# Performance work log

Hardware: AMD Instinct MI355X
Metric: run time of the kernel (lower is better)

## Reference

```python
import jax, jax.numpy as jnp
import numpy as np

T = 8
TAU = 2.0
V_TH = 1.0
V_RESET = 0.0
ALPHA = 2.0  # ATan surrogate alpha

@jax.custom_vjp
def spike(v):
    # Heaviside(v) with ATan surrogate gradient
    return (v >= 0.0).astype(v.dtype)

def _spike_fwd(v):
    return spike(v), v

def _spike_bwd(v, g):
    sg = (ALPHA / 2.0) / (1.0 + (jnp.pi / 2.0 * ALPHA * v) ** 2)
    return (g * sg,)

spike.defvjp(_spike_fwd, _spike_bwd)

def conv2d(x, w):
    return jax.lax.conv_general_dilated(x, w, (1, 1), 'SAME',
                                        dimension_numbers=('NCHW', 'OIHW', 'NCHW'))

def batchnorm(x, g, b, m, v):
    # inference-mode BN over channel dim of NCHW
    scale = (g / jnp.sqrt(v + 1e-5))[None, :, None, None]
    return (x - m[None, :, None, None]) * scale + b[None, :, None, None]

def maxpool2(x):
    return jax.lax.reduce_window(x, -jnp.inf, jax.lax.max,
                                 (1, 1, 2, 2), (1, 1, 2, 2), 'VALID')

def if_scan(x_seq):
    # x_seq: [T, ...]; IF neuron: v += x; spike; hard reset
    def step(v, x_t):
        v = v + x_t
        s = spike(v - V_TH)
        v = v * (1.0 - s) + V_RESET * s
        return v, s
    v0 = jnp.full_like(x_seq[0], V_RESET)
    _, s_seq = jax.lax.scan(step, v0, x_seq)
    return s_seq

def lif_scan(x_seq):
    # LIF neuron: v += (x - (v - v_reset)) / tau; spike; hard reset
    def step(v, x_t):
        v = v + (x_t - (v - V_RESET)) / TAU
        s = spike(v - V_TH)
        v = v * (1.0 - s) + V_RESET * s
        return v, s
    v0 = jnp.full_like(x_seq[0], V_RESET)
    _, s_seq = jax.lax.scan(step, v0, x_seq)
    return s_seq

def setup_inputs() -> dict:
    key = jax.random.key(0)
    ks = jax.random.split(key, 6)
    B = 64
    d = {
        'x': jax.random.normal(ks[0], (B, 1, 28, 28), dtype=jnp.float32),
        'conv1_w': jax.random.normal(ks[1], (128, 1, 3, 3), dtype=jnp.float32) * 0.3,
        'bn1_g': jnp.ones((128,), jnp.float32),
        'bn1_b': jnp.zeros((128,), jnp.float32),
        'bn1_m': jnp.zeros((128,), jnp.float32),
        'bn1_v': jnp.ones((128,), jnp.float32),
        'conv2_w': jax.random.normal(ks[2], (128, 128, 3, 3), dtype=jnp.float32) * 0.05,
        'bn2_g': jnp.ones((128,), jnp.float32),
        'bn2_b': jnp.zeros((128,), jnp.float32),
        'bn2_m': jnp.zeros((128,), jnp.float32),
        'bn2_v': jnp.ones((128,), jnp.float32),
        'fc1_w': jax.random.normal(ks[3], (128 * 3 * 3, 128 * 7 * 7), dtype=jnp.float32) * 0.02,
        'fc2_w': jax.random.normal(ks[4], (128, 128 * 3 * 3), dtype=jnp.float32) * 0.05,
        'fc3_w': jax.random.normal(ks[5], (10, 128), dtype=jnp.float32) * 0.1,
    }
    return d

def reference(x, conv1_w, bn1_g, bn1_b, bn1_m, bn1_v,
              conv2_w, bn2_g, bn2_b, bn2_m, bn2_v,
              fc1_w, fc2_w, fc3_w):
    B = x.shape[0]
    # static conv + BN (applied once, repeated T times)
    y0 = batchnorm(conv2d(x, conv1_w), bn1_g, bn1_b, bn1_m, bn1_v)  # [B,128,28,28]
    x_seq = jnp.broadcast_to(y0, (T,) + y0.shape)
    s1 = if_scan(x_seq)  # [T,B,128,28,28]
    # pool -> conv -> BN per timestep (vectorized over T*B)
    h = s1.reshape((T * B, 128, 28, 28))
    h = maxpool2(h)                       # [TB,128,14,14]
    h = batchnorm(conv2d(h, conv2_w), bn2_g, bn2_b, bn2_m, bn2_v)
    s2 = if_scan(h.reshape((T, B, 128, 14, 14)))
    # pool -> flatten (dropout is identity in eval mode)
    h = maxpool2(s2.reshape((T * B, 128, 14, 14)))  # [TB,128,7,7]
    h = h.reshape((T, B, 128 * 7 * 7))
    h = jnp.einsum('tbi,oi->tbo', h, fc1_w)   # [T,B,1152]
    s3 = lif_scan(h)
    h = jnp.einsum('tbi,oi->tbo', s3, fc2_w)  # [T,B,128]
    s4 = lif_scan(h)
    h = jnp.einsum('tbi,oi->tbo', s4, fc3_w)  # [T,B,10]
    s5 = lif_scan(h)
    return s5.sum(0) / T
```

## Files before the change

### kernel.cpp

```cpp
#include <hip/hip_runtime.h>
#include <hip/hip_bf16.h>
#include <cstddef>


typedef __attribute__((ext_vector_type(8))) short  short8;
typedef __attribute__((ext_vector_type(4))) float  f32x4;
typedef __attribute__((ext_vector_type(8))) __bf16 bf16x8;

__device__ inline short f2bf_bits(float x) {
    __hip_bfloat16 h = __float2bfloat16(x);
    return *reinterpret_cast<short*>(&h);
}
__device__ inline float bfbits2f(short b) {
    __hip_bfloat16 h;
    *reinterpret_cast<short*>(&h) = b;
    return __bfloat162float(h);
}

__global__ __launch_bounds__(256) void prep2_kernel(
    const float* __restrict__ w2, const float* __restrict__ g2,
    const float* __restrict__ v2, __hip_bfloat16* __restrict__ w2s,
    float* __restrict__ sc2)
{
    int id = blockIdx.x * 256 + threadIdx.x;
    if (id < 128) sc2[id] = g2[id] / sqrtf(v2[id] + 1e-5f);
    int ci = id & 127;
    int co = (id >> 7) & 127;
    int k  = id >> 14;
    float w  = w2[(co * 128 + ci) * 9 + k];
    float hi = __bfloat162float(__float2bfloat16(w));
    float r1 = w - hi;
    float md = __bfloat162float(__float2bfloat16(r1));
    float r2 = r1 - md;
    size_t base = ((size_t)k * 128 + co) * 128 + ci;
    const size_t SPL = 9 * 128 * 128;
    w2s[0 * SPL + base] = __float2bfloat16(hi);
    w2s[1 * SPL + base] = __float2bfloat16(md);
    w2s[2 * SPL + base] = __float2bfloat16(r2);
}

__global__ __launch_bounds__(256) void prep_fc1_kernel(
    const float* __restrict__ w, short* __restrict__ w1s)
{
    int id = blockIdx.x * 256 + threadIdx.x;
    int koct = id % 784;
    int n    = id / 784;
    const float* src = w + (size_t)n * 6272 + koct * 8;
    float4 va = *(const float4*)src;
    float4 vb = *(const float4*)(src + 4);
    float wv[8] = {va.x, va.y, va.z, va.w, vb.x, vb.y, vb.z, vb.w};
    short8 hi8, md8, lo8;
#pragma unroll
    for (int e = 0; e < 8; ++e) {
        float x  = wv[e];
        short hb = f2bf_bits(x);
        float r1 = x - bfbits2f(hb);
        short mb = f2bf_bits(r1);
        float r2 = r1 - bfbits2f(mb);
        hi8[e] = hb; md8[e] = mb; lo8[e] = f2bf_bits(r2);
    }
    const size_t SPL = (size_t)1152 * 6272;
    size_t base = (size_t)n * 6272 + koct * 8;
    *(short8*)&w1s[0 * SPL + base] = hi8;
    *(short8*)&w1s[1 * SPL + base] = md8;
    *(short8*)&w1s[2 * SPL + base] = lo8;
}

__global__ __launch_bounds__(256) void stage1_kernel(
    const float* __restrict__ x,  const float* __restrict__ w1,
    const float* __restrict__ g1, const float* __restrict__ b1,
    const float* __restrict__ m1, const float* __restrict__ v1,
    __hip_bfloat16* __restrict__ p1bf)
{
    int id = blockIdx.x * 256 + threadIdx.x;
    int c  = id & 127;
    int bp = id >> 7;
    int p  = bp % 196;
    int b  = bp / 196;
    int ph = p / 14, pw = p % 14;

    float scale = g1[c] / sqrtf(v1[c] + 1e-5f);
    float mu = m1[c], beta = b1[c];
    float wl[9];
#pragma unroll
    for (int k = 0; k < 9; ++k) wl[k] = w1[c * 9 + k];

    const float* xb = x + b * 784;
    float y[4];
#pragma unroll
    for (int i = 0; i < 4; ++i) {
        int h = 2 * ph + (i >> 1);
        int w = 2 * pw + (i & 1);
        float acc = 0.f;
#pragma unroll
        for (int kh = 0; kh < 3; ++kh) {
#pragma unroll
            for (int kw = 0; kw < 3; ++kw) {
                int hh = h + kh - 1, ww = w + kw - 1;
                if ((unsigned)hh < 28u && (unsigned)ww < 28u)
                    acc += xb[hh * 28 + ww] * wl[kh * 3 + kw];
            }
        }
        y[i] = (acc - mu) * scale + beta;
    }

    float v0 = 0.f, v1m = 0.f, v2m = 0.f, v3m = 0.f;
#pragma unroll
    for (int t = 0; t < 8; ++t) {
        float any = 0.f;
        v0  += y[0]; if (v0  >= 1.0f) { any = 1.0f; v0  = 0.0f; }
        v1m += y[1]; if (v1m >= 1.0f) { any = 1.0f; v1m = 0.0f; }
        v2m += y[2]; if (v2m >= 1.0f) { any = 1.0f; v2m = 0.0f; }
        v3m += y[3]; if (v3m >= 1.0f) { any = 1.0f; v3m = 0.0f; }
        p1bf[((size_t)(t * 64 + b) * 196 + p) * 128 + c] = __float2bfloat16(any);
    }
}

__global__ __launch_bounds__(256, 2) void conv2m_kernel(
    const short* __restrict__ p1bf, const short* __restrict__ w2s,
    const float* __restrict__ sc2,  const float* __restrict__ b2,
    const float* __restrict__ m2,   float* __restrict__ a2t)
{
    __shared__ short patch[272 * 128];
    int bx   = blockIdx.x;
    int tb   = bx >> 1;
    int ch   = bx & 1;
    int tid  = threadIdx.x;
    int lane = tid & 63;
    int wv   = tid >> 6;
    int wm   = wv >> 1, wn = wv & 1;
    int l15  = lane & 15, lg = lane >> 4;

    const short8 z8 = {0, 0, 0, 0, 0, 0, 0, 0};
    for (int idx = tid; idx < 76 * 16; idx += 256) {
        int cell = idx >> 4, sl = idx & 15;
        int prow, pcol;
        if (cell < 48) {
            int g = cell >> 4;
            prow = (g == 0) ? 0 : ((g == 1) ? 15 : 16);
            pcol = cell & 15;
        } else {
            int e = cell - 48;
            prow = 1 + (e >> 1);
            pcol = (e & 1) ? 15 : 0;
        }
        *(short8*)&patch[(prow * 16 + pcol) * 128 + sl * 8] = z8;
    }
    const short* src = p1bf + (size_t)tb * (196 * 128);
    for (int idx = tid; idx < 196 * 16; idx += 256) {
        int pos = idx >> 4, q = idx & 15;
        short8 v = *(const short8*)&src[pos * 128 + q * 8];
        int h = pos / 14, w = pos - h * 14;
        int lpos = (h + 1) * 16 + (w + 1);
        *(short8*)&patch[lpos * 128 + (q ^ (lpos & 15)) * 8] = v;
    }
    __syncthreads();

    int abase[7];
#pragma unroll
    for (int mi = 0; mi < 7; ++mi) {
        int pos = (wm * 6 + mi) * 16 + l15;
        int r = pos / 14, c = pos - r * 14;
        abase[mi] = r * 16 + c;
    }
    int co0 = ch * 64 + wn * 32;

    f32x4 acc[7][2];
#pragma unroll
    for (int mi = 0; mi < 7; ++mi) {
        acc[mi][0] = (f32x4){0.f, 0.f, 0.f, 0.f};
        acc[mi][1] = (f32x4){0.f, 0.f, 0.f, 0.f};
    }

    const size_t SPL = 9 * 128 * 128;
    for (int chunk = 0; chunk < 4; ++chunk) {
#pragma unroll
        for (int tap = 0; tap < 9; ++tap) {
            const int t16 = (tap / 3) * 16 + (tap % 3);
            short8 bfr[3][2];
#pragma unroll
            for (int s = 0; s < 3; ++s)
#pragma unroll
                for (int nt = 0; nt < 2; ++nt)
                    bfr[s][nt] = *(const short8*)&w2s[s * SPL +
                        ((size_t)tap * 128 + co0 + nt * 16 + l15) * 128 + chunk * 32 + lg * 8];
#pragma unroll
            for (int mi = 0; mi < 7; ++mi) {
                int lpos = abase[mi] + t16;
                short8 av = *(const short8*)&patch[lpos * 128 +
                                                   (((chunk * 4 + lg) ^ (lpos & 15)) * 8)];
                if (wm == 1 && mi == 6 && l15 >= 4) av = z8;
                bf16x8 a = __builtin_bit_cast(bf16x8, av);
#pragma unroll
                for (int s = 0; s < 3; ++s)
#pragma unroll
                    for (int nt = 0; nt < 2; ++nt)
                        acc[mi][nt] = __builtin_amdgcn_mfma_f32_16x16x32_bf16(
                            a, __builtin_bit_cast(bf16x8, bfr[s][nt]), acc[mi][nt], 0, 0, 0);
            }
        }
    }

    float scv[2], mv[2], bv[2];
#pragma unroll
    for (int nt = 0; nt < 2; ++nt) {
        int co = co0 + nt * 16 + l15;
        scv[nt] = sc2[co]; mv[nt] = m2[co]; bv[nt] = b2[co];
    }
#pragma unroll
    for (int mi = 0; mi < 7; ++mi) {
        int mt = wm * 6 + mi;
#pragma unroll
        for (int nt = 0; nt < 2; ++nt) {
            int co = co0 + nt * 16 + l15;
#pragma unroll
            for (int reg = 0; reg < 4; ++reg) {
                int pos = mt * 16 + lg * 4 + reg;
                if (pos < 196)
                    a2t[((size_t)tb * 196 + pos) * 128 + co] =
                        (acc[mi][nt][reg] - mv[nt]) * scv[nt] + bv[nt];
            }
        }
    }
}

__global__ __launch_bounds__(256) void stage2_kernel(
    const float* __restrict__ a2t, __hip_bfloat16* __restrict__ p2)
{
    int id = blockIdx.x * 256 + threadIdx.x;
    int c  = id & 127;
    int bp = id >> 7;
    int p  = bp % 49;
    int b  = bp / 49;
    int ph = p / 7, pw = p % 7;
    int s0 = (2 * ph) * 14 + 2 * pw;

    float v0 = 0.f, v1 = 0.f, v2 = 0.f, v3 = 0.f;
#pragma unroll
    for (int t = 0; t < 8; ++t) {
        const float* base = a2t + ((size_t)(t * 64 + b) * 196) * 128 + c;
        float x0 = base[(s0) * 128],      x1 = base[(s0 + 1) * 128];
        float x2 = base[(s0 + 14) * 128], x3 = base[(s0 + 15) * 128];
        float any = 0.f;
        v0 += x0; if (v0 >= 1.0f) { any = 1.0f; v0 = 0.0f; }
        v1 += x1; if (v1 >= 1.0f) { any = 1.0f; v1 = 0.0f; }
        v2 += x2; if (v2 >= 1.0f) { any = 1.0f; v2 = 0.0f; }
        v3 += x3; if (v3 >= 1.0f) { any = 1.0f; v3 = 0.0f; }
        p2[(size_t)(t * 64 + b) * 6272 + c * 49 + p] = __float2bfloat16(any);
    }
}

__global__ __launch_bounds__(256, 2) void fc1m_kernel(
    const short* __restrict__ A,
    const short* __restrict__ Bsp,
    float* __restrict__ part)
{
    __shared__ short At[64 * 64];
    const int n0 = blockIdx.x * 128;
    const int m0 = blockIdx.y * 64;
    const int kz = blockIdx.z;
    const int tid  = threadIdx.x;
    const int lane = tid & 63;
    const int wv   = tid >> 6;
    const int wm = wv >> 1, wn = wv & 1;
    const int l15 = lane & 15, lg = lane >> 4;
    const size_t SPL = (size_t)1152 * 6272;

    f32x4 acc[2][4];
#pragma unroll
    for (int mi = 0; mi < 2; ++mi)
#pragma unroll
        for (int nt = 0; nt < 4; ++nt)
            acc[mi][nt] = (f32x4){0.f, 0.f, 0.f, 0.f};

    for (int ks = 0; ks < 14; ++ks) {
        int k0 = kz * 896 + ks * 64;
#pragma unroll
        for (int pp = 0; pp < 2; ++pp) {
            int i = pp * 256 + tid;
            int row = i >> 3, q = i & 7;
            short8 v = *(const short8*)&A[(size_t)(m0 + row) * 6272 + k0 + ((q ^ (row & 7)) << 3)];
            *(short8*)&At[row * 64 + q * 8] = v;
        }
        __syncthreads();

#pragma unroll
        for (int kh = 0; kh < 2; ++kh) {
            bf16x8 a[2];
#pragma unroll
            for (int mi = 0; mi < 2; ++mi) {
                int r = wm * 32 + mi * 16 + l15;
                int q = (kh * 4 + lg) ^ (r & 7);
                a[mi] = __builtin_bit_cast(bf16x8, *(const short8*)&At[r * 64 + q * 8]);
            }
#pragma unroll
            for (int s = 0; s < 3; ++s) {
#pragma unroll
                for (int nt = 0; nt < 4; ++nt) {
                    bf16x8 b = __builtin_bit_cast(bf16x8, *(const short8*)&Bsp[s * SPL +
                        (size_t)(n0 + wn * 64 + nt * 16 + l15) * 6272 + k0 + kh * 32 + lg * 8]);
                    acc[0][nt] = __builtin_amdgcn_mfma_f32_16x16x32_bf16(a[0], b, acc[0][nt], 0, 0, 0);
                    acc[1][nt] = __builtin_amdgcn_mfma_f32_16x16x32_bf16(a[1], b, acc[1][nt], 0, 0, 0);
                }
            }
        }
        __syncthreads();
    }

    float* dst = part + (size_t)kz * (512 * 1152);
#pragma unroll
    for (int mi = 0; mi < 2; ++mi) {
#pragma unroll
        for (int nt = 0; nt < 4; ++nt) {
            int n = n0 + wn * 64 + nt * 16 + l15;
#pragma unroll
            for (int reg = 0; reg < 4; ++reg) {
                int m = m0 + wm * 32 + mi * 16 + lg * 4 + reg;
                dst[(size_t)m * 1152 + n] = acc[mi][nt][reg];
            }
        }
    }
}

__global__ __launch_bounds__(256) void lif2_kernel(
    const float* __restrict__ part, float* __restrict__ s3)
{
    int id = blockIdx.x * 256 + threadIdx.x;
    int f = id % 1152;
    int b = id / 1152;
    const size_t S = (size_t)512 * 1152;
    float v = 0.f;
#pragma unroll
    for (int t = 0; t < 8; ++t) {
        size_t off = (size_t)(t * 64 + b) * 1152 + f;
        float x = part[off];
#pragma unroll
        for (int s = 1; s < 7; ++s) x += part[s * S + off];
        v = v + (x - v) * 0.5f;
        s3[off] = (v >= 1.0f) ? 1.0f : 0.0f;
        if (v >= 1.0f) v = 0.0f;
    }
}

__global__ __launch_bounds__(256) void gemm_nt_kernel(
    const float* __restrict__ A, const float* __restrict__ Bw,
    float* __restrict__ C, int M, int N, int K)
{
    __shared__ float As[16][36];
    __shared__ float Bs[16][68];
    int m_base = blockIdx.y * 32;
    int n_base = blockIdx.x * 64;
    int tid = threadIdx.x;
    int tx = tid & 15, ty = tid >> 4;
    float acc[2][4] = {{0.f,0.f,0.f,0.f},{0.f,0.f,0.f,0.f}};

    for (int k0 = 0; k0 < K; k0 += 16) {
        if (tid < 128) {
            int m  = tid >> 2;
            int kk = (tid & 3) << 2;
            float4 av = *(const float4*)&A[(size_t)(m_base + m) * K + k0 + kk];
            As[kk + 0][m] = av.x; As[kk + 1][m] = av.y;
            As[kk + 2][m] = av.z; As[kk + 3][m] = av.w;
        }
        {
            int n  = tid >> 2;
            int kk = (tid & 3) << 2;
            float4 bv = *(const float4*)&Bw[(size_t)(n_base + n) * K + k0 + kk];
            Bs[kk + 0][n] = bv.x; Bs[kk + 1][n] = bv.y;
            Bs[kk + 2][n] = bv.z; Bs[kk + 3][n] = bv.w;
        }
        __syncthreads();
#pragma unroll
        for (int kk = 0; kk < 16; ++kk) {
            float a0 = As[kk][ty * 2 + 0];
            float a1 = As[kk][ty * 2 + 1];
            float4 bv = *(const float4*)&Bs[kk][tx * 4];
            acc[0][0] += a0 * bv.x; acc[0][1] += a0 * bv.y;
            acc[0][2] += a0 * bv.z; acc[0][3] += a0 * bv.w;
            acc[1][0] += a1 * bv.x; acc[1][1] += a1 * bv.y;
            acc[1][2] += a1 * bv.z; acc[1][3] += a1 * bv.w;
        }
        __syncthreads();
    }
#pragma unroll
    for (int i = 0; i < 2; ++i) {
        float4 r;
        r.x = acc[i][0]; r.y = acc[i][1]; r.z = acc[i][2]; r.w = acc[i][3];
        *(float4*)&C[(size_t)(m_base + ty * 2 + i) * N + n_base + tx * 4] = r;
    }
}

__global__ __launch_bounds__(128) void tail_kernel(
    const float* __restrict__ h2, const float* __restrict__ w3,
    float* __restrict__ out)
{
    __shared__ float st[8][128];
    __shared__ float dd[8][10];
    int b = blockIdx.x;
    int tid = threadIdx.x;
    float v = 0.f;
#pragma unroll
    for (int t = 0; t < 8; ++t) {
        float x = h2[(size_t)(t * 64 + b) * 128 + tid];
        v = v + (x - v) * 0.5f;
        st[t][tid] = (v >= 1.0f) ? 1.0f : 0.0f;
        if (v >= 1.0f) v = 0.0f;
    }
    __syncthreads();
    if (tid < 80) {
        int t = tid / 10, o = tid - (tid / 10) * 10;
        float dot = 0.f;
        for (int k = 0; k < 128; ++k) dot += st[t][k] * w3[o * 128 + k];
        dd[t][o] = dot;
    }
    __syncthreads();
    if (tid < 10) {
        float vv = 0.f, cnt = 0.f;
#pragma unroll
        for (int t = 0; t < 8; ++t) {
            float x = dd[t][tid];
            vv = vv + (x - vv) * 0.5f;
            if (vv >= 1.0f) { cnt += 1.0f; vv = 0.0f; }
        }
        out[b * 10 + tid] = cnt * 0.125f;
    }
}

extern "C" void kernel_launch(void* const* d_in, const int* in_sizes, int n_in,
                              void* d_out, int out_size, void* d_ws, size_t ws_size,
                              hipStream_t stream)
{
    (void)in_sizes; (void)n_in; (void)out_size; (void)ws_size;
    const float* x    = (const float*)d_in[0];
    const float* w1   = (const float*)d_in[1];
    const float* g1   = (const float*)d_in[2];
    const float* b1   = (const float*)d_in[3];
    const float* m1   = (const float*)d_in[4];
    const float* v1   = (const float*)d_in[5];
    const float* w2   = (const float*)d_in[6];
    const float* g2   = (const float*)d_in[7];
    const float* b2   = (const float*)d_in[8];
    const float* m2   = (const float*)d_in[9];
    const float* v2   = (const float*)d_in[10];
    const float* fc1w = (const float*)d_in[11];
    const float* fc2w = (const float*)d_in[12];
    const float* fc3w = (const float*)d_in[13];
    float* out = (float*)d_out;

    char* ws = (char*)d_ws;
    __hip_bfloat16* p1bf = (__hip_bfloat16*)(ws + 0);
    float*          a2t  = (float*)(ws + 25690112);
    __hip_bfloat16* w2s  = (__hip_bfloat16*)(ws + 77070336);
    float*          sc2  = (float*)(ws + 77955072);
    __hip_bfloat16* p2bf = (__hip_bfloat16*)(ws + 0);
    float*          part = (float*)(ws + 6422528);
    float*          s3   = (float*)(ws + 22937600);
    float*          h2   = (float*)(ws + 25296896);
    short*          w1s  = (short*)(ws + 25690112);

    prep2_kernel  <<<576,  256, 0, stream>>>(w2, g2, v2, w2s, sc2);
    stage1_kernel <<<6272, 256, 0, stream>>>(x, w1, g1, b1, m1, v1, p1bf);
    conv2m_kernel <<<1024, 256, 0, stream>>>((const short*)p1bf, (const short*)w2s,
                                             sc2, b2, m2, a2t);
    stage2_kernel <<<1568, 256, 0, stream>>>(a2t, p2bf);
    prep_fc1_kernel<<<3528, 256, 0, stream>>>(fc1w, w1s);
    fc1m_kernel   <<<dim3(9, 8, 7), 256, 0, stream>>>((const short*)p2bf, w1s, part);
    lif2_kernel   <<<288,  256, 0, stream>>>(part, s3);
    gemm_nt_kernel<<<dim3(2, 16), 256, 0, stream>>>(s3, fc2w, h2, 512, 128, 1152);
    tail_kernel   <<<64,   128, 0, stream>>>(h2, fc3w, out);
}
```

Before: 466.2 us.

## Halve conv2 LDS tile, swap fc1 grid order, fuse fc2 GEMM with LIF tail

The conv2 kernel now stages the input patch in two 64-channel halves, halving shared memory so the occupancy hint can rise from 2 to 4 blocks per SM. It swaps the XOR swizzle to use 8 slots. The fc1 grid is transposed so adjacent blocks walk M instead of N, which changes L2 reuse of the weights. The fp32 fc2 GEMM and the tail kernel are replaced by one fused kernel per batch element that reads bf16 spikes and does a 3-way bf16 split of fc2 weights on MFMA. That removes a launch and the h2 round trip, but the conversion is redone in every block.

Result: faster. 439.1 us (-5.8%).

```diff
diff --git a/kernel.cpp b/kernel.cpp
--- a/kernel.cpp
+++ b/kernel.cpp
@@ -116,12 +116,12 @@
     }
 }
 
-__global__ __launch_bounds__(256, 2) void conv2m_kernel(
+__global__ __launch_bounds__(256, 4) void conv2m_kernel(
     const short* __restrict__ p1bf, const short* __restrict__ w2s,
     const float* __restrict__ sc2,  const float* __restrict__ b2,
     const float* __restrict__ m2,   float* __restrict__ a2t)
 {
-    __shared__ short patch[272 * 128];
+    __shared__ short patch[272 * 64];
     int bx   = blockIdx.x;
     int tb   = bx >> 1;
     int ch   = bx & 1;
@@ -132,8 +132,8 @@
     int l15  = lane & 15, lg = lane >> 4;
 
     const short8 z8 = {0, 0, 0, 0, 0, 0, 0, 0};
-    for (int idx = tid; idx < 76 * 16; idx += 256) {
-        int cell = idx >> 4, sl = idx & 15;
+    for (int idx = tid; idx < 76 * 8; idx += 256) {
+        int cell = idx >> 3, q = idx & 7;
         int prow, pcol;
         if (cell < 48) {
             int g = cell >> 4;
@@ -144,24 +144,16 @@
             prow = 1 + (e >> 1);
             pcol = (e & 1) ? 15 : 0;
         }
-        *(short8*)&patch[(prow * 16 + pcol) * 128 + sl * 8] = z8;
-    }
-    const short* src = p1bf + (size_t)tb * (196 * 128);
-    for (int idx = tid; idx < 196 * 16; idx += 256) {
-        int pos = idx >> 4, q = idx & 15;
-        short8 v = *(const short8*)&src[pos * 128 + q * 8];
-        int h = pos / 14, w = pos - h * 14;
-        int lpos = (h + 1) * 16 + (w + 1);
-        *(short8*)&patch[lpos * 128 + (q ^ (lpos & 15)) * 8] = v;
-    }
-    __syncthreads();
-
-    int abase[7];
+        *(short8*)&patch[(prow * 16 + pcol) * 64 + q * 8] = z8;
+    }
+
+    int abase[7], pbase[7];
 #pragma unroll
     for (int mi = 0; mi < 7; ++mi) {
         int pos = (wm * 6 + mi) * 16 + l15;
         int r = pos / 14, c = pos - r * 14;
         abase[mi] = r * 16 + c;
+        pbase[mi] = pos;
     }
     int co0 = ch * 64 + wn * 32;
 
@@ -172,31 +164,47 @@
         acc[mi][1] = (f32x4){0.f, 0.f, 0.f, 0.f};
     }
 
+    const short* src = p1bf + (size_t)tb * (196 * 128);
     const size_t SPL = 9 * 128 * 128;
-    for (int chunk = 0; chunk < 4; ++chunk) {
-#pragma unroll
-        for (int tap = 0; tap < 9; ++tap) {
-            const int t16 = (tap / 3) * 16 + (tap % 3);
-            short8 bfr[3][2];
-#pragma unroll
-            for (int s = 0; s < 3; ++s)
-#pragma unroll
-                for (int nt = 0; nt < 2; ++nt)
-                    bfr[s][nt] = *(const short8*)&w2s[s * SPL +
-                        ((size_t)tap * 128 + co0 + nt * 16 + l15) * 128 + chunk * 32 + lg * 8];
-#pragma unroll
-            for (int mi = 0; mi < 7; ++mi) {
-                int lpos = abase[mi] + t16;
-                short8 av = *(const short8*)&patch[lpos * 128 +
-                                                   (((chunk * 4 + lg) ^ (lpos & 15)) * 8)];
-                if (wm == 1 && mi == 6 && l15 >= 4) av = z8;
-                bf16x8 a = __builtin_bit_cast(bf16x8, av);
+
+    for (int half = 0; half < 2; ++half) {
+        if (half) __syncthreads();
+        for (int idx = tid; idx < 196 * 8; idx += 256) {
+            int pos = idx >> 3, q = idx & 7;
+            short8 v = *(const short8*)&src[pos * 128 + half * 64 + q * 8];
+            int h = pos / 14, w = pos - h * 14;
+            int lpos = (h + 1) * 16 + (w + 1);
+            *(short8*)&patch[lpos * 64 + ((q ^ (pos & 7)) << 3)] = v;
+        }
+        __syncthreads();
+
+        for (int c2 = 0; c2 < 2; ++c2) {
+            int cibase = half * 64 + c2 * 32;
+#pragma unroll
+            for (int tap = 0; tap < 9; ++tap) {
+                const int t16 = (tap / 3) * 16 + (tap % 3);
+                const int tc  = (tap / 3 - 1) * 14 + (tap % 3) - 1;
+                short8 bfr[3][2];
 #pragma unroll
                 for (int s = 0; s < 3; ++s)
 #pragma unroll
                     for (int nt = 0; nt < 2; ++nt)
-                        acc[mi][nt] = __builtin_amdgcn_mfma_f32_16x16x32_bf16(
-                            a, __builtin_bit_cast(bf16x8, bfr[s][nt]), acc[mi][nt], 0, 0, 0);
+                        bfr[s][nt] = *(const short8*)&w2s[s * SPL +
+                            ((size_t)tap * 128 + co0 + nt * 16 + l15) * 128 + cibase + lg * 8];
+#pragma unroll
+                for (int mi = 0; mi < 7; ++mi) {
+                    int lpos = abase[mi] + t16;
+                    int q2 = (c2 * 4 + lg) ^ ((pbase[mi] + tc) & 7);
+                    short8 av = *(const short8*)&patch[lpos * 64 + q2 * 8];
+                    if (wm == 1 && mi == 6 && l15 >= 4) av = z8;
+                    bf16x8 a = __builtin_bit_cast(bf16x8, av);
+#pragma unroll
+                    for (int s = 0; s < 3; ++s)
+#pragma unroll
+                        for (int nt = 0; nt < 2; ++nt)
+                            acc[mi][nt] = __builtin_amdgcn_mfma_f32_16x16x32_bf16(
+                                a, __builtin_bit_cast(bf16x8, bfr[s][nt]), acc[mi][nt], 0, 0, 0);
+                }
             }
         }
     }
@@ -256,8 +264,8 @@
     float* __restrict__ part)
 {
     __shared__ short At[64 * 64];
-    const int n0 = blockIdx.x * 128;
-    const int m0 = blockIdx.y * 64;
+    const int m0 = blockIdx.x * 64;
+    const int n0 = blockIdx.y * 128;
     const int kz = blockIdx.z;
     const int tid  = threadIdx.x;
     const int lane = tid & 63;
@@ -323,7 +331,7 @@
 }
 
 __global__ __launch_bounds__(256) void lif2_kernel(
-    const float* __restrict__ part, float* __restrict__ s3)
+    const float* __restrict__ part, __hip_bfloat16* __restrict__ s3)
 {
     int id = blockIdx.x * 256 + threadIdx.x;
     int f = id % 1152;
@@ -337,80 +345,84 @@
 #pragma unroll
         for (int s = 1; s < 7; ++s) x += part[s * S + off];
         v = v + (x - v) * 0.5f;
-        s3[off] = (v >= 1.0f) ? 1.0f : 0.0f;
+        s3[off] = __float2bfloat16((v >= 1.0f) ? 1.0f : 0.0f);
         if (v >= 1.0f) v = 0.0f;
     }
 }
 
-__global__ __launch_bounds__(256) void gemm_nt_kernel(
-    const float* __restrict__ A, const float* __restrict__ Bw,
-    float* __restrict__ C, int M, int N, int K)
-{
-    __shared__ float As[16][36];
-    __shared__ float Bs[16][68];
-    int m_base = blockIdx.y * 32;
-    int n_base = blockIdx.x * 64;
-    int tid = threadIdx.x;
-    int tx = tid & 15, ty = tid >> 4;
-    float acc[2][4] = {{0.f,0.f,0.f,0.f},{0.f,0.f,0.f,0.f}};
-
-    for (int k0 = 0; k0 < K; k0 += 16) {
-        if (tid < 128) {
-            int m  = tid >> 2;
-            int kk = (tid & 3) << 2;
-            float4 av = *(const float4*)&A[(size_t)(m_base + m) * K + k0 + kk];
-            As[kk + 0][m] = av.x; As[kk + 1][m] = av.y;
-            As[kk + 2][m] = av.z; As[kk + 3][m] = av.w;
-        }
-        {
-            int n  = tid >> 2;
-            int kk = (tid & 3) << 2;
-            float4 bv = *(const float4*)&Bw[(size_t)(n_base + n) * K + k0 + kk];
-            Bs[kk + 0][n] = bv.x; Bs[kk + 1][n] = bv.y;
-            Bs[kk + 2][n] = bv.z; Bs[kk + 3][n] = bv.w;
-        }
-        __syncthreads();
-#pragma unroll
-        for (int kk = 0; kk < 16; ++kk) {
-            float a0 = As[kk][ty * 2 + 0];
-            float a1 = As[kk][ty * 2 + 1];
-            float4 bv = *(const float4*)&Bs[kk][tx * 4];
-            acc[0][0] += a0 * bv.x; acc[0][1] += a0 * bv.y;
-            acc[0][2] += a0 * bv.z; acc[0][3] += a0 * bv.w;
-            acc[1][0] += a1 * bv.x; acc[1][1] += a1 * bv.y;
-            acc[1][2] += a1 * bv.z; acc[1][3] += a1 * bv.w;
-        }
-        __syncthreads();
-    }
-#pragma unroll
-    for (int i = 0; i < 2; ++i) {
-        float4 r;
-        r.x = acc[i][0]; r.y = acc[i][1]; r.z = acc[i][2]; r.w = acc[i][3];
-        *(float4*)&C[(size_t)(m_base + ty * 2 + i) * N + n_base + tx * 4] = r;
-    }
-}
-
-__global__ __launch_bounds__(128) void tail_kernel(
-    const float* __restrict__ h2, const float* __restrict__ w3,
+__global__ __launch_bounds__(256) void fc2tail_kernel(
+    const short* __restrict__ s3bf,
+    const float* __restrict__ fc2w,
+    const float* __restrict__ fc3w,
     float* __restrict__ out)
 {
-    __shared__ float st[8][128];
+    __shared__ float h2[8][128];
+    __shared__ float s4[8][128];
     __shared__ float dd[8][10];
-    int b = blockIdx.x;
-    int tid = threadIdx.x;
-    float v = 0.f;
-#pragma unroll
-    for (int t = 0; t < 8; ++t) {
-        float x = h2[(size_t)(t * 64 + b) * 128 + tid];
-        v = v + (x - v) * 0.5f;
-        st[t][tid] = (v >= 1.0f) ? 1.0f : 0.0f;
-        if (v >= 1.0f) v = 0.0f;
+    int b    = blockIdx.x;
+    int tid  = threadIdx.x;
+    int lane = tid & 63;
+    int wv   = tid >> 6;
+    int l15  = lane & 15, lg = lane >> 4;
+
+    const short8 z8 = {0, 0, 0, 0, 0, 0, 0, 0};
+    f32x4 acc[2] = {(f32x4){0.f, 0.f, 0.f, 0.f}, (f32x4){0.f, 0.f, 0.f, 0.f}};
+
+    for (int ks = 0; ks < 36; ++ks) {
+        short8 av = (l15 < 8)
+            ? *(const short8*)&s3bf[(size_t)(l15 * 64 + b) * 1152 + ks * 32 + lg * 8]
+            : z8;
+        bf16x8 a = __builtin_bit_cast(bf16x8, av);
+#pragma unroll
+        for (int nt = 0; nt < 2; ++nt) {
+            int o = wv * 32 + nt * 16 + l15;
+            const float* wp = &fc2w[(size_t)o * 1152 + ks * 32 + lg * 8];
+            float4 wa = *(const float4*)wp;
+            float4 wb = *(const float4*)(wp + 4);
+            float wvv[8] = {wa.x, wa.y, wa.z, wa.w, wb.x, wb.y, wb.z, wb.w};
+            short8 hi8, md8, lo8;
+#pragma unroll
+            for (int e = 0; e < 8; ++e) {
+                float xw = wvv[e];
+                short hb = f2bf_bits(xw);
+                float r1 = xw - bfbits2f(hb);
+                short mb = f2bf_bits(r1);
+                float r2 = r1 - bfbits2f(mb);
+                hi8[e] = hb; md8[e] = mb; lo8[e] = f2bf_bits(r2);
+            }
+            acc[nt] = __builtin_amdgcn_mfma_f32_16x16x32_bf16(
+                a, __builtin_bit_cast(bf16x8, hi8), acc[nt], 0, 0, 0);
+            acc[nt] = __builtin_amdgcn_mfma_f32_16x16x32_bf16(
+                a, __builtin_bit_cast(bf16x8, md8), acc[nt], 0, 0, 0);
+            acc[nt] = __builtin_amdgcn_mfma_f32_16x16x32_bf16(
+                a, __builtin_bit_cast(bf16x8, lo8), acc[nt], 0, 0, 0);
+        }
+    }
+#pragma unroll
+    for (int nt = 0; nt < 2; ++nt) {
+#pragma unroll
+        for (int reg = 0; reg < 4; ++reg) {
+            int t = lg * 4 + reg;
+            if (t < 8) h2[t][wv * 32 + nt * 16 + l15] = acc[nt][reg];
+        }
+    }
+    __syncthreads();
+
+    if (tid < 128) {
+        float v = 0.f;
+#pragma unroll
+        for (int t = 0; t < 8; ++t) {
+            float xv = h2[t][tid];
+            v = v + (xv - v) * 0.5f;
+            s4[t][tid] = (v >= 1.0f) ? 1.0f : 0.0f;
+            if (v >= 1.0f) v = 0.0f;
+        }
     }
     __syncthreads();
     if (tid < 80) {
         int t = tid / 10, o = tid - (tid / 10) * 10;
         float dot = 0.f;
-        for (int k = 0; k < 128; ++k) dot += st[t][k] * w3[o * 128 + k];
+        for (int k = 0; k < 128; ++k) dot += s4[t][k] * fc3w[o * 128 + k];
         dd[t][o] = dot;
     }
     __syncthreads();
@@ -418,8 +430,8 @@
         float vv = 0.f, cnt = 0.f;
 #pragma unroll
         for (int t = 0; t < 8; ++t) {
-            float x = dd[t][tid];
-            vv = vv + (x - vv) * 0.5f;
+            float xv = dd[t][tid];
+            vv = vv + (xv - vv) * 0.5f;
             if (vv >= 1.0f) { cnt += 1.0f; vv = 0.0f; }
         }
         out[b * 10 + tid] = cnt * 0.125f;
@@ -454,18 +466,16 @@
     float*          sc2  = (float*)(ws + 77955072);
     __hip_bfloat16* p2bf = (__hip_bfloat16*)(ws + 0);
     float*          part = (float*)(ws + 6422528);
-    float*          s3   = (float*)(ws + 22937600);
-    float*          h2   = (float*)(ws + 25296896);
+    __hip_bfloat16* s3bf = (__hip_bfloat16*)(ws + 22937600);
     short*          w1s  = (short*)(ws + 25690112);
 
-    prep2_kernel  <<<576,  256, 0, stream>>>(w2, g2, v2, w2s, sc2);
-    stage1_kernel <<<6272, 256, 0, stream>>>(x, w1, g1, b1, m1, v1, p1bf);
-    conv2m_kernel <<<1024, 256, 0, stream>>>((const short*)p1bf, (const short*)w2s,
-                                             sc2, b2, m2, a2t);
-    stage2_kernel <<<1568, 256, 0, stream>>>(a2t, p2bf);
+    prep2_kernel   <<<576,  256, 0, stream>>>(w2, g2, v2, w2s, sc2);
+    stage1_kernel  <<<6272, 256, 0, stream>>>(x, w1, g1, b1, m1, v1, p1bf);
+    conv2m_kernel  <<<1024, 256, 0, stream>>>((const short*)p1bf, (const short*)w2s,
+                                              sc2, b2, m2, a2t);
+    stage2_kernel  <<<1568, 256, 0, stream>>>(a2t, p2bf);
     prep_fc1_kernel<<<3528, 256, 0, stream>>>(fc1w, w1s);
-    fc1m_kernel   <<<dim3(9, 8, 7), 256, 0, stream>>>((const short*)p2bf, w1s, part);
-    lif2_kernel   <<<288,  256, 0, stream>>>(part, s3);
-    gemm_nt_kernel<<<dim3(2, 16), 256, 0, stream>>>(s3, fc2w, h2, 512, 128, 1152);
-    tail_kernel   <<<64,   128, 0, stream>>>(h2, fc3w, out);
-}
+    fc1m_kernel    <<<dim3(8, 9, 7), 256, 0, stream>>>((const short*)p2bf, w1s, part);
+    lif2_kernel    <<<288,  256, 0, stream>>>(part, s3bf);
+    fc2tail_kernel <<<64,   256, 0, stream>>>((const short*)s3bf, fc2w, fc3w, out);
+}
```
